# Kernel optimization log

Measured on AMD Instinct MI355X. Metric: run time of the kernel, lower is better.

Reference implementation:

```python
import jax, jax.numpy as jnp
import numpy as np

SIZE = 1024
LATENT_DIM = 256
BETA_C = 0.25
LEGACY = True


def setup_inputs() -> dict:
    key = jax.random.key(0)
    k1, k2 = jax.random.split(key)
    z = jax.random.normal(k1, (8, LATENT_DIM, 16, 16, 16), dtype=jnp.float32)
    # nn.Embedding weight initialized uniform(-1/size, 1/size)
    embedding = jax.random.uniform(
        k2, (SIZE, LATENT_DIM), minval=-1.0 / SIZE, maxval=1.0 / SIZE, dtype=jnp.float32
    )
    return {"z": z, "embedding": embedding}


def reference(z, embedding):
    sg = jax.lax.stop_gradient
    B, C, D, H, W = z.shape
    # [B, D, H, W, C]
    zp = jnp.transpose(z, (0, 2, 3, 4, 1))
    zf = zp.reshape(-1, C)  # [N, C]
    # pairwise squared distances [N, K]
    d = (
        jnp.sum(zf * zf, axis=1, keepdims=True)
        + jnp.sum(embedding * embedding, axis=1)
        - 2.0 * (zf @ embedding.T)
    )
    idx = jnp.argmin(d, axis=1)  # [N]
    # direct gather == one-hot @ embedding
    z_q = embedding[idx].reshape(zp.shape)
    if LEGACY:
        loss = jnp.mean((sg(z_q) - zp) ** 2) + BETA_C * jnp.mean((z_q - sg(zp)) ** 2)
    else:
        loss = BETA_C * jnp.mean((sg(z_q) - zp) ** 2) + jnp.mean((z_q - sg(zp)) ** 2)
    # perplexity: e_mean = mean of one-hot encodings == normalized counts
    counts = jnp.zeros((SIZE,), dtype=z.dtype).at[idx].add(1.0)
    e_mean = counts / zf.shape[0]
    perplexity = jnp.exp(-jnp.sum(e_mean * jnp.log(e_mean + 1e-10)))
    # straight-through estimator
    z_q = zp + sg(z_q - zp)
    z_q = jnp.transpose(z_q, (0, 4, 1, 2, 3))  # back to [B, C, D, H, W]
    return z_q, loss, perplexity, idx
```

## Files before the change

kernel.cpp:

```cpp
#include <hip/hip_runtime.h>
#include <cstddef>
#include <cstdint>

#define CDIM 256
#define SPAT 4096
#define KCODE 1024

#define LOSS_OFF 8388608
#define PERP_OFF 8388609
#define IDX_OFF  8388610

typedef __bf16 bf16x8 __attribute__((ext_vector_type(8)));
typedef float floatx16 __attribute__((ext_vector_type(16)));
typedef unsigned short ushort8 __attribute__((ext_vector_type(8)));

__device__ __forceinline__ unsigned short f2bf_rne(float f) {
    union { float f; uint32_t u; } c; c.f = f;
    uint32_t u = c.u;
    return (unsigned short)((u + 0x7fffu + ((u >> 16) & 1u)) >> 16);
}
__device__ __forceinline__ float bf2f(unsigned short h) {
    union { float f; uint32_t u; } c; c.u = ((uint32_t)h) << 16;
    return c.f;
}

__device__ __forceinline__ void dma16(const void* g, void* l) {
    __builtin_amdgcn_global_load_lds(
        (const __attribute__((address_space(1))) void*)g,
        (__attribute__((address_space(3))) void*)l, 16, 0, 0);
}

__global__ __launch_bounds__(256) void vq_prep(const float* __restrict__ emb,
                                               unsigned short* __restrict__ ehsw,
                                               unsigned short* __restrict__ elsw,
                                               float* __restrict__ enorm,
                                               float* __restrict__ counts,
                                               float* __restrict__ losssum) {
    int tid = threadIdx.x;
    if (blockIdx.x == 0) {
        for (int i = tid; i < KCODE; i += 256) counts[i] = 0.0f;
        if (tid == 0) losssum[0] = 0.0f;
    }
    int w = tid >> 6, lane = tid & 63;
    int k = blockIdx.x * 4 + w;
    const float* row = emb + (size_t)k * CDIM;
    float s = 0.0f;
#pragma unroll
    for (int i = 0; i < 4; ++i) {
        float v = row[lane + 64 * i];
        s = fmaf(v, v, s);
    }
#pragma unroll
    for (int m = 32; m > 0; m >>= 1) s += __shfl_xor(s, m, 64);
    if (lane == 0) enorm[k] = s;

    float4 v4 = *(const float4*)(row + lane * 4);
    unsigned short h0 = f2bf_rne(v4.x), h1 = f2bf_rne(v4.y),
                   h2 = f2bf_rne(v4.z), h3 = f2bf_rne(v4.w);
    ushort4 hv = make_ushort4(h0, h1, h2, h3);
    ushort4 lv = make_ushort4(f2bf_rne(v4.x - bf2f(h0)), f2bf_rne(v4.y - bf2f(h1)),
                              f2bf_rne(v4.z - bf2f(h2)), f2bf_rne(v4.w - bf2f(h3)));
    int kb = lane >> 1, cj = (lane & 1) * 4;
    int st = k >> 5, ks = k & 31;
    int phys = kb ^ (ks & 7);
    size_t dst = (size_t)st * 8192 + ks * 256 + phys * 8 + cj;
    *(ushort4*)(ehsw + dst) = hv;
    *(ushort4*)(elsw + dst) = lv;
}

__global__ __launch_bounds__(512, 2) void vq_main(const float* __restrict__ z,
                                                  const float* __restrict__ emb,
                                                  const unsigned short* __restrict__ ehsw,
                                                  const unsigned short* __restrict__ elsw,
                                                  const float* __restrict__ enorm,
                                                  float* __restrict__ counts,
                                                  float* __restrict__ losssum,
                                                  float* __restrict__ out) {
    __shared__ __align__(16) unsigned char lds[131072 + 4096 + 512 + 1024 + 1024 + 512];
    float* zhalf = (float*)lds;
    float* ens_s = (float*)(lds + 131072);
    float* zzs   = (float*)(lds + 135168);
    float* pb_s  = (float*)(lds + 135680);
    int*   pb_i  = (int*)(lds + 136704);
    int*   bidxs = (int*)(lds + 137728);

    const int tid = threadIdx.x;
    const int w = tid >> 6;
    const int lane = tid & 63;
    const int m_ = lane & 31;
    const int g = lane >> 5;
    const int kh = w >> 2;
    const int cq = w & 3;
    const int ch = cq & 1;
    const int hlf = cq >> 1;
    const int n0 = blockIdx.x * 128;
    const int b = n0 >> 12;
    const int sp0 = n0 & 4095;
    const float* zb = z + (size_t)b * CDIM * SPAT + sp0;

    ushort8 zh[16], zl[16];

    for (int h = 0; h < 2; ++h) {
        for (int i = tid; i < CDIM * 16; i += 512) {
            int c = i >> 4, seg = i & 15;
            *(float4*)&zhalf[c * 64 + seg * 4] =
                *(const float4*)(zb + (size_t)c * SPAT + h * 64 + seg * 4);
        }
        __syncthreads();
        if (hlf == h) {
#pragma unroll
            for (int kc = 0; kc < 16; ++kc) {
#pragma unroll
                for (int j = 0; j < 8; ++j) {
                    float v = zhalf[(kc * 16 + g * 8 + j) * 64 + ch * 32 + m_];
                    unsigned short hb = f2bf_rne(v);
                    unsigned short lb = f2bf_rne(v - bf2f(hb));
                    zh[kc][j] = hb; zl[kc][j] = lb;
                }
            }
        } else if (w == (h == 0 ? 2 : 0)) {
            float s = 0.0f;
            for (int c = 0; c < CDIM; ++c) {
                float v = zhalf[c * 64 + lane];
                s = fmaf(v, v, s);
            }
            zzs[h * 64 + lane] = s;
        } else if (h == 0 && w == 3) {
            for (int i = lane; i < KCODE; i += 64) ens_s[i] = enorm[i];
        }
        __syncthreads();
    }

    const float zzv = zzs[cq * 32 + m_];

    float bs = 3.4e38f;
    int bi_ = 0;

    const int bufid = w >> 1;
    const int hf = w & 1;
    const char* gsrc = (const char*)((bufid & 1) ? elsw : ehsw);
    const int gs0 = kh * 16;

    {
        const char* gp = gsrc + ((size_t)gs0 << 14) + (hf << 13) + (lane << 4);
        char* lp = (char*)lds + ((size_t)bufid << 14) + (hf << 13);
#pragma unroll
        for (int j = 0; j < 8; ++j) dma16(gp + j * 1024, lp + j * 1024);
    }

    for (int s = 0; s < 16; ++s) {
        __syncthreads();
        if (s < 15) {
            const char* gp = gsrc + ((size_t)(gs0 + s + 1) << 14) + (hf << 13) + (lane << 4);
            char* lp = (char*)lds + (((size_t)(s + 1) & 1) << 16) +
                       ((size_t)bufid << 14) + (hf << 13);
#pragma unroll
            for (int j = 0; j < 8; ++j) dma16(gp + j * 1024, lp + j * 1024);
            __builtin_amdgcn_sched_barrier(0);
        }
        const char* EHb = (const char*)lds + (((size_t)s & 1) << 16) + ((size_t)kh << 15);
        const char* ELb = EHb + 16384;

        floatx16 a = {0.0f, 0.0f, 0.0f, 0.0f, 0.0f, 0.0f, 0.0f, 0.0f,
                      0.0f, 0.0f, 0.0f, 0.0f, 0.0f, 0.0f, 0.0f, 0.0f};
#pragma unroll
        for (int kc = 0; kc < 16; ++kc) {
            int kb0 = kc * 2 + g;
            int off = m_ * 512 + ((kb0 ^ (m_ & 7)) << 4);
            bf16x8 aeh = *(const bf16x8*)(EHb + off);
            bf16x8 ael = *(const bf16x8*)(ELb + off);
            bf16x8 bh = __builtin_bit_cast(bf16x8, zh[kc]);
            bf16x8 bl = __builtin_bit_cast(bf16x8, zl[kc]);
            a = __builtin_amdgcn_mfma_f32_32x32x16_bf16(aeh, bh, a, 0, 0, 0);
            a = __builtin_amdgcn_mfma_f32_32x32x16_bf16(ael, bh, a, 0, 0, 0);
            a = __builtin_amdgcn_mfma_f32_32x32x16_bf16(aeh, bl, a, 0, 0, 0);
        }

#pragma unroll
        for (int reg = 0; reg < 16; ++reg) {
            int mm = (reg & 3) + 8 * (reg >> 2) + 4 * g;
            int code = kh * 512 + s * 32 + mm;
            float en = ens_s[code];
            float d = (zzv + en) - 2.0f * a[reg];
            if (d < bs) { bs = d; bi_ = code; }
        }
    }

    {
        float s2 = __shfl_xor(bs, 32, 64);
        int i2 = __shfl_xor(bi_, 32, 64);
        if (s2 < bs || (s2 == bs && i2 < bi_)) { bs = s2; bi_ = i2; }
    }
    __syncthreads();
    if (lane < 32) {
        pb_s[kh * 128 + cq * 32 + m_] = bs;
        pb_i[kh * 128 + cq * 32 + m_] = bi_;
    }
    __syncthreads();
    if (tid < 128) {
        float s0 = pb_s[tid], s1 = pb_s[128 + tid];
        int i0 = pb_i[tid], i1 = pb_i[128 + tid];
        int ki = (s1 < s0) ? i1 : i0;
        bidxs[tid] = ki;
        out[IDX_OFF + n0 + tid] = (float)ki;
        atomicAdd(&counts[ki], 1.0f);
    }
    __syncthreads();

#pragma unroll
    for (int r = 0; r < 16; ++r) {
        int row = w * 16 + r;
        int k = bidxs[row];
        int slot = (row & 3) * 32 + (row >> 2);
        dma16((const char*)emb + ((size_t)k << 10) + (lane << 4),
              (char*)lds + (size_t)slot * 1040);
    }
    __syncthreads();

    if (tid < 256) {
        float ls = 0.0f;
        float* outz = out + (size_t)b * CDIM * SPAT + sp0;
        const int col4 = tid & 31;
        const int c_0 = tid >> 5;
        const float* e0 = (const float*)((const char*)lds + (size_t)(0 * 32 + col4) * 1040);
        const float* e1 = (const float*)((const char*)lds + (size_t)(1 * 32 + col4) * 1040);
        const float* e2 = (const float*)((const char*)lds + (size_t)(2 * 32 + col4) * 1040);
        const float* e3 = (const float*)((const char*)lds + (size_t)(3 * 32 + col4) * 1040);
        for (int c = c_0; c < CDIM; c += 8) {
            float4 zp = *(const float4*)(zb + (size_t)c * SPAT + col4 * 4);
            float d0 = e0[c] - zp.x, d1 = e1[c] - zp.y,
                  d2 = e2[c] - zp.z, d3 = e3[c] - zp.w;
            float4 o;
            o.x = zp.x + d0; o.y = zp.y + d1; o.z = zp.z + d2; o.w = zp.w + d3;
            ls = fmaf(d0, d0, ls); ls = fmaf(d1, d1, ls);
            ls = fmaf(d2, d2, ls); ls = fmaf(d3, d3, ls);
            *(float4*)(outz + (size_t)c * SPAT + col4 * 4) = o;
        }
#pragma unroll
        for (int m = 32; m > 0; m >>= 1) ls += __shfl_xor(ls, m, 64);
        if (lane == 0) atomicAdd(losssum, ls);
    }
}

__global__ __launch_bounds__(256) void vq_finalize(const float* __restrict__ counts,
                                                   const float* __restrict__ losssum,
                                                   float* __restrict__ out) {
    __shared__ float red[256];
    int tid = threadIdx.x;
    float s = 0.0f;
    for (int k = tid; k < KCODE; k += 256) {
        float em = counts[k] * (1.0f / 32768.0f);
        s += em * logf(em + 1e-10f);
    }
    red[tid] = s;
    __syncthreads();
    for (int off = 128; off > 0; off >>= 1) {
        if (tid < off) red[tid] += red[tid + off];
        __syncthreads();
    }
    if (tid == 0) {
        float m = losssum[0] * (1.0f / 8388608.0f);
        out[LOSS_OFF] = m + 0.25f * m;
        out[PERP_OFF] = expf(-red[0]);
    }
}

extern "C" void kernel_launch(void* const* d_in, const int* in_sizes, int n_in,
                              void* d_out, int out_size, void* d_ws, size_t ws_size,
                              hipStream_t stream) {
    const float* z = (const float*)d_in[0];
    const float* emb = (const float*)d_in[1];
    float* out = (float*)d_out;
    unsigned short* ehsw = (unsigned short*)d_ws;
    unsigned short* elsw = ehsw + (size_t)KCODE * CDIM;
    float* enorm = (float*)(elsw + (size_t)KCODE * CDIM);
    float* counts = enorm + KCODE;
    float* losssum = counts + KCODE;

    vq_prep<<<256, 256, 0, stream>>>(emb, ehsw, elsw, enorm, counts, losssum);
    vq_main<<<256, 512, 0, stream>>>(z, emb, ehsw, elsw, enorm, counts, losssum, out);
    vq_finalize<<<1, 256, 0, stream>>>(counts, losssum, out);
}
```

Baseline: 157.5 us.

## Stage z in LDS and stream codebook fragments directly from global into registers

The z tile is now converted to bf16 hi/lo pairs and stored swizzled in LDS, where every warp reads it. The codebook is pre-laid out in MFMA fragment order and loaded straight from global memory into registers. This removes the double-buffered DMA pipeline and its per-stage barriers. Each warp now computes a 2x2 register tile of 32x32 MFMA blocks so each loaded fragment is reused twice. The code-chunk start is rotated by block id to spread L2 traffic, and the final argmin merge goes from 2 to 4 partials. The cost is much higher global/L2 read traffic for codebook fragments, which now have no LDS staging or prefetch, and more accumulator registers.

After: 197.3 us. 1.25x slower.

```diff
diff --git a/kernel.cpp b/kernel.cpp
--- a/kernel.cpp
+++ b/kernel.cpp
@@ -30,9 +30,11 @@
         (__attribute__((address_space(3))) void*)l, 16, 0, 0);
 }
 
+#define MFMA32(A, B, C) __builtin_amdgcn_mfma_f32_32x32x16_bf16((A), (B), (C), 0, 0, 0)
+
 __global__ __launch_bounds__(256) void vq_prep(const float* __restrict__ emb,
-                                               unsigned short* __restrict__ ehsw,
-                                               unsigned short* __restrict__ elsw,
+                                               unsigned short* __restrict__ abt_h,
+                                               unsigned short* __restrict__ abt_l,
                                                float* __restrict__ enorm,
                                                float* __restrict__ counts,
                                                float* __restrict__ losssum) {
@@ -60,147 +62,148 @@
     ushort4 hv = make_ushort4(h0, h1, h2, h3);
     ushort4 lv = make_ushort4(f2bf_rne(v4.x - bf2f(h0)), f2bf_rne(v4.y - bf2f(h1)),
                               f2bf_rne(v4.z - bf2f(h2)), f2bf_rne(v4.w - bf2f(h3)));
-    int kb = lane >> 1, cj = (lane & 1) * 4;
-    int st = k >> 5, ks = k & 31;
-    int phys = kb ^ (ks & 7);
-    size_t dst = (size_t)st * 8192 + ks * 256 + phys * 8 + cj;
-    *(ushort4*)(ehsw + dst) = hv;
-    *(ushort4*)(elsw + dst) = lv;
+    size_t dst = (size_t)(k >> 5) * 8192 + (lane >> 2) * 512 + (k & 31) * 16 +
+                 ((lane >> 1) & 1) * 8 + (lane & 1) * 4;
+    *(ushort4*)(abt_h + dst) = hv;
+    *(ushort4*)(abt_l + dst) = lv;
 }
 
 __global__ __launch_bounds__(512, 2) void vq_main(const float* __restrict__ z,
                                                   const float* __restrict__ emb,
-                                                  const unsigned short* __restrict__ ehsw,
-                                                  const unsigned short* __restrict__ elsw,
+                                                  const unsigned short* __restrict__ abt_h,
+                                                  const unsigned short* __restrict__ abt_l,
                                                   const float* __restrict__ enorm,
                                                   float* __restrict__ counts,
                                                   float* __restrict__ losssum,
                                                   float* __restrict__ out) {
-    __shared__ __align__(16) unsigned char lds[131072 + 4096 + 512 + 1024 + 1024 + 512];
-    float* zhalf = (float*)lds;
+    __shared__ __align__(16) unsigned char lds[140288];
     float* ens_s = (float*)(lds + 131072);
     float* zzs   = (float*)(lds + 135168);
     float* pb_s  = (float*)(lds + 135680);
-    int*   pb_i  = (int*)(lds + 136704);
-    int*   bidxs = (int*)(lds + 137728);
+    int*   pb_i  = (int*)(lds + 137728);
+    int*   bidxs = (int*)(lds + 139776);
 
     const int tid = threadIdx.x;
     const int w = tid >> 6;
     const int lane = tid & 63;
     const int m_ = lane & 31;
     const int g = lane >> 5;
-    const int kh = w >> 2;
-    const int cq = w & 3;
-    const int ch = cq & 1;
-    const int hlf = cq >> 1;
-    const int n0 = blockIdx.x * 128;
+    const int bid = blockIdx.x;
+    const int n0 = bid * 128;
     const int b = n0 >> 12;
     const int sp0 = n0 & 4095;
     const float* zb = z + (size_t)b * CDIM * SPAT + sp0;
 
-    ushort8 zh[16], zl[16];
-
-    for (int h = 0; h < 2; ++h) {
-        for (int i = tid; i < CDIM * 16; i += 512) {
-            int c = i >> 4, seg = i & 15;
-            *(float4*)&zhalf[c * 64 + seg * 4] =
-                *(const float4*)(zb + (size_t)c * SPAT + h * 64 + seg * 4);
-        }
-        __syncthreads();
-        if (hlf == h) {
-#pragma unroll
-            for (int kc = 0; kc < 16; ++kc) {
+    if (tid < 384) {
+#pragma unroll
+        for (int it = 0; it < 11; ++it) {
+            int task = tid + it * 384;
+            if (task < 4096) {
+                int col = task & 127, chunk = task >> 7;
+                ushort8 hv, lv;
 #pragma unroll
                 for (int j = 0; j < 8; ++j) {
-                    float v = zhalf[(kc * 16 + g * 8 + j) * 64 + ch * 32 + m_];
-                    unsigned short hb = f2bf_rne(v);
-                    unsigned short lb = f2bf_rne(v - bf2f(hb));
-                    zh[kc][j] = hb; zl[kc][j] = lb;
+                    float f = zb[(size_t)(chunk * 8 + j) * SPAT + col];
+                    unsigned short hb = f2bf_rne(f);
+                    hv[j] = hb;
+                    lv[j] = f2bf_rne(f - bf2f(hb));
                 }
+                int baddr = (col * 512 + chunk * 16) ^ ((col & 7) << 4);
+                *(ushort8*)(lds + baddr) = hv;
+                *(ushort8*)(lds + 65536 + baddr) = lv;
             }
-        } else if (w == (h == 0 ? 2 : 0)) {
-            float s = 0.0f;
-            for (int c = 0; c < CDIM; ++c) {
-                float v = zhalf[c * 64 + lane];
-                s = fmaf(v, v, s);
-            }
-            zzs[h * 64 + lane] = s;
-        } else if (h == 0 && w == 3) {
-            for (int i = lane; i < KCODE; i += 64) ens_s[i] = enorm[i];
-        }
-        __syncthreads();
-    }
-
-    const float zzv = zzs[cq * 32 + m_];
-
-    float bs = 3.4e38f;
-    int bi_ = 0;
-
-    const int bufid = w >> 1;
-    const int hf = w & 1;
-    const char* gsrc = (const char*)((bufid & 1) ? elsw : ehsw);
-    const int gs0 = kh * 16;
-
-    {
-        const char* gp = gsrc + ((size_t)gs0 << 14) + (hf << 13) + (lane << 4);
-        char* lp = (char*)lds + ((size_t)bufid << 14) + (hf << 13);
-#pragma unroll
-        for (int j = 0; j < 8; ++j) dma16(gp + j * 1024, lp + j * 1024);
-    }
-
-    for (int s = 0; s < 16; ++s) {
-        __syncthreads();
-        if (s < 15) {
-            const char* gp = gsrc + ((size_t)(gs0 + s + 1) << 14) + (hf << 13) + (lane << 4);
-            char* lp = (char*)lds + (((size_t)(s + 1) & 1) << 16) +
-                       ((size_t)bufid << 14) + (hf << 13);
-#pragma unroll
-            for (int j = 0; j < 8; ++j) dma16(gp + j * 1024, lp + j * 1024);
-            __builtin_amdgcn_sched_barrier(0);
-        }
-        const char* EHb = (const char*)lds + (((size_t)s & 1) << 16) + ((size_t)kh << 15);
-        const char* ELb = EHb + 16384;
-
-        floatx16 a = {0.0f, 0.0f, 0.0f, 0.0f, 0.0f, 0.0f, 0.0f, 0.0f,
-                      0.0f, 0.0f, 0.0f, 0.0f, 0.0f, 0.0f, 0.0f, 0.0f};
+        }
+    } else {
+        int col = tid - 384;
+        float s = 0.0f;
+        for (int c = 0; c < CDIM; ++c) {
+            float v = zb[(size_t)c * SPAT + col];
+            s = fmaf(v, v, s);
+        }
+        zzs[col] = s;
+    }
+    for (int i = tid; i < KCODE; i += 512) ens_s[i] = enorm[i];
+    __syncthreads();
+
+    const int cq8 = w >> 1;
+    const int cv = w & 1;
+    const int aoff = m_ * 32 + g * 16;
+    const int col0 = cv * 64 + m_;
+    const int col1 = col0 + 32;
+    const int swz = (col0 & 7) << 4;
+    const int bo0 = col0 * 512 + g * 16;
+    const int bo1 = col1 * 512 + g * 16;
+    const float zzv0 = zzs[col0], zzv1 = zzs[col1];
+
+    float bs0 = 3.4e38f, bs1 = 3.4e38f;
+    int bi0 = 0, bi1 = 0;
+
+    const floatx16 z16 = {0.0f, 0.0f, 0.0f, 0.0f, 0.0f, 0.0f, 0.0f, 0.0f,
+                          0.0f, 0.0f, 0.0f, 0.0f, 0.0f, 0.0f, 0.0f, 0.0f};
+
+    for (int cpi = 0; cpi < 4; ++cpi) {
+        const int cp = (cpi + bid) & 3;
+        const int blkA = cq8 * 8 + cp * 2;
+        const int blkB = blkA + 1;
+        const char* pAh = (const char*)abt_h + ((size_t)blkA << 14) + aoff;
+        const char* pAl = (const char*)abt_l + ((size_t)blkA << 14) + aoff;
+        const char* pBh = (const char*)abt_h + ((size_t)blkB << 14) + aoff;
+        const char* pBl = (const char*)abt_l + ((size_t)blkB << 14) + aoff;
+        floatx16 a00 = z16, a01 = z16, a10 = z16, a11 = z16;
 #pragma unroll
         for (int kc = 0; kc < 16; ++kc) {
-            int kb0 = kc * 2 + g;
-            int off = m_ * 512 + ((kb0 ^ (m_ & 7)) << 4);
-            bf16x8 aeh = *(const bf16x8*)(EHb + off);
-            bf16x8 ael = *(const bf16x8*)(ELb + off);
-            bf16x8 bh = __builtin_bit_cast(bf16x8, zh[kc]);
-            bf16x8 bl = __builtin_bit_cast(bf16x8, zl[kc]);
-            a = __builtin_amdgcn_mfma_f32_32x32x16_bf16(aeh, bh, a, 0, 0, 0);
-            a = __builtin_amdgcn_mfma_f32_32x32x16_bf16(ael, bh, a, 0, 0, 0);
-            a = __builtin_amdgcn_mfma_f32_32x32x16_bf16(aeh, bl, a, 0, 0, 0);
-        }
-
+            bf16x8 aeh0 = *(const bf16x8*)(pAh + kc * 1024);
+            bf16x8 ael0 = *(const bf16x8*)(pAl + kc * 1024);
+            bf16x8 aeh1 = *(const bf16x8*)(pBh + kc * 1024);
+            bf16x8 ael1 = *(const bf16x8*)(pBl + kc * 1024);
+            bf16x8 bh0 = *(const bf16x8*)(lds + ((bo0 + kc * 32) ^ swz));
+            bf16x8 bl0 = *(const bf16x8*)(lds + 65536 + ((bo0 + kc * 32) ^ swz));
+            bf16x8 bh1 = *(const bf16x8*)(lds + ((bo1 + kc * 32) ^ swz));
+            bf16x8 bl1 = *(const bf16x8*)(lds + 65536 + ((bo1 + kc * 32) ^ swz));
+            a00 = MFMA32(aeh0, bh0, a00); a00 = MFMA32(ael0, bh0, a00); a00 = MFMA32(aeh0, bl0, a00);
+            a01 = MFMA32(aeh0, bh1, a01); a01 = MFMA32(ael0, bh1, a01); a01 = MFMA32(aeh0, bl1, a01);
+            a10 = MFMA32(aeh1, bh0, a10); a10 = MFMA32(ael1, bh0, a10); a10 = MFMA32(aeh1, bl0, a10);
+            a11 = MFMA32(aeh1, bh1, a11); a11 = MFMA32(ael1, bh1, a11); a11 = MFMA32(aeh1, bl1, a11);
+        }
 #pragma unroll
         for (int reg = 0; reg < 16; ++reg) {
             int mm = (reg & 3) + 8 * (reg >> 2) + 4 * g;
-            int code = kh * 512 + s * 32 + mm;
-            float en = ens_s[code];
-            float d = (zzv + en) - 2.0f * a[reg];
-            if (d < bs) { bs = d; bi_ = code; }
+            int code0 = blkA * 32 + mm, code1 = blkB * 32 + mm;
+            float en0 = ens_s[code0], en1 = ens_s[code1];
+            float d;
+            d = (zzv0 + en0) - 2.0f * a00[reg];
+            if (d < bs0 || (d == bs0 && code0 < bi0)) { bs0 = d; bi0 = code0; }
+            d = (zzv1 + en0) - 2.0f * a01[reg];
+            if (d < bs1 || (d == bs1 && code0 < bi1)) { bs1 = d; bi1 = code0; }
+            d = (zzv0 + en1) - 2.0f * a10[reg];
+            if (d < bs0 || (d == bs0 && code1 < bi0)) { bs0 = d; bi0 = code1; }
+            d = (zzv1 + en1) - 2.0f * a11[reg];
+            if (d < bs1 || (d == bs1 && code1 < bi1)) { bs1 = d; bi1 = code1; }
         }
     }
 
     {
-        float s2 = __shfl_xor(bs, 32, 64);
-        int i2 = __shfl_xor(bi_, 32, 64);
-        if (s2 < bs || (s2 == bs && i2 < bi_)) { bs = s2; bi_ = i2; }
-    }
-    __syncthreads();
+        float s2 = __shfl_xor(bs0, 32, 64);
+        int i2 = __shfl_xor(bi0, 32, 64);
+        if (s2 < bs0 || (s2 == bs0 && i2 < bi0)) { bs0 = s2; bi0 = i2; }
+        float s3 = __shfl_xor(bs1, 32, 64);
+        int i3 = __shfl_xor(bi1, 32, 64);
+        if (s3 < bs1 || (s3 == bs1 && i3 < bi1)) { bs1 = s3; bi1 = i3; }
+    }
     if (lane < 32) {
-        pb_s[kh * 128 + cq * 32 + m_] = bs;
-        pb_i[kh * 128 + cq * 32 + m_] = bi_;
+        pb_s[cq8 * 128 + col0] = bs0; pb_i[cq8 * 128 + col0] = bi0;
+        pb_s[cq8 * 128 + col1] = bs1; pb_i[cq8 * 128 + col1] = bi1;
     }
     __syncthreads();
     if (tid < 128) {
-        float s0 = pb_s[tid], s1 = pb_s[128 + tid];
-        int i0 = pb_i[tid], i1 = pb_i[128 + tid];
-        int ki = (s1 < s0) ? i1 : i0;
+        float s = pb_s[tid];
+        int ki = pb_i[tid];
+#pragma unroll
+        for (int q = 1; q < 4; ++q) {
+            float s2 = pb_s[q * 128 + tid];
+            int i2 = pb_i[q * 128 + tid];
+            if (s2 < s || (s2 == s && i2 < ki)) { s = s2; ki = i2; }
+        }
         bidxs[tid] = ki;
         out[IDX_OFF + n0 + tid] = (float)ki;
         atomicAdd(&counts[ki], 1.0f);
@@ -222,10 +225,10 @@
         float* outz = out + (size_t)b * CDIM * SPAT + sp0;
         const int col4 = tid & 31;
         const int c_0 = tid >> 5;
-        const float* e0 = (const float*)((const char*)lds + (size_t)(0 * 32 + col4) * 1040);
-        const float* e1 = (const float*)((const char*)lds + (size_t)(1 * 32 + col4) * 1040);
-        const float* e2 = (const float*)((const char*)lds + (size_t)(2 * 32 + col4) * 1040);
-        const float* e3 = (const float*)((const char*)lds + (size_t)(3 * 32 + col4) * 1040);
+        const float* e0 = (const float*)(lds + (size_t)(0 * 32 + col4) * 1040);
+        const float* e1 = (const float*)(lds + (size_t)(1 * 32 + col4) * 1040);
+        const float* e2 = (const float*)(lds + (size_t)(2 * 32 + col4) * 1040);
+        const float* e3 = (const float*)(lds + (size_t)(3 * 32 + col4) * 1040);
         for (int c = c_0; c < CDIM; c += 8) {
             float4 zp = *(const float4*)(zb + (size_t)c * SPAT + col4 * 4);
             float d0 = e0[c] - zp.x, d1 = e1[c] - zp.y,
@@ -271,13 +274,14 @@
     const float* z = (const float*)d_in[0];
     const float* emb = (const float*)d_in[1];
     float* out = (float*)d_out;
-    unsigned short* ehsw = (unsigned short*)d_ws;
-    unsigned short* elsw = ehsw + (size_t)KCODE * CDIM;
-    float* enorm = (float*)(elsw + (size_t)KCODE * CDIM);
+    unsigned short* abt_h = (unsigned short*)d_ws;
+    unsigned short* abt_l = abt_h + (size_t)KCODE * CDIM;
+    float* enorm = (float*)(abt_l + (size_t)KCODE * CDIM);
     float* counts = enorm + KCODE;
     float* losssum = counts + KCODE;
 
-    vq_prep<<<256, 256, 0, stream>>>(emb, ehsw, elsw, enorm, counts, losssum);
-    vq_main<<<256, 512, 0, stream>>>(z, emb, ehsw, elsw, enorm, counts, losssum, out);
+    vq_prep<<<256, 256, 0, stream>>>(emb, abt_h, abt_l, enorm, counts, losssum);
+    vq_main<<<256, 512, 0, stream>>>(z, emb, abt_h, abt_l, enorm,
+                                     counts, losssum, out);
     vq_finalize<<<1, 256, 0, stream>>>(counts, losssum, out);
 }
```
